# Kernel optimization log

Measured on AMD Instinct MI355X. Metric: run time of the kernel, lower is better.

## Reference

```python
import jax, jax.numpy as jnp
import numpy as np

DIM = 1024
L = 10
C = 1.0
SQRT_C = float(np.sqrt(C))


def _exp_map(x, v, c):
    # Poincare exp map (general form, as in the torch source)
    xn2 = jnp.sum(x * x, axis=-1, keepdims=True)
    lam = 2.0 / (1.0 - c * xn2)
    vn = jnp.sqrt(jnp.sum(v * v, axis=-1, keepdims=True))
    vn = jnp.maximum(vn, 1e-8)
    second = jnp.tanh(SQRT_C * lam * vn / 2.0) / (SQRT_C * vn) * v
    num = (1.0 - c * xn2) * second
    den = (1.0 - 2.0 * c * jnp.sum(x * second, axis=-1, keepdims=True)
           + c * c * xn2 * jnp.sum(second * second, axis=-1, keepdims=True))
    return x + num / den


def _log_map(x, y, c):
    # Poincare log map (general form, as in the torch source)
    xn2 = jnp.sum(x * x, axis=-1, keepdims=True)
    lam = 2.0 / (1.0 - c * xn2)
    yn2 = jnp.sum(y * y, axis=-1, keepdims=True)
    xy = jnp.sum(x * y, axis=-1, keepdims=True)
    tv = (-x * yn2 + y * (1.0 + c * xn2) - 2.0 * c * xy * x) / (1.0 - c * xn2)
    tn = jnp.sqrt(jnp.sum(tv * tv, axis=-1, keepdims=True))
    num = 2.0 * SQRT_C * jnp.arctanh(SQRT_C * tn)
    den = SQRT_C * lam * tn
    return num / den * tv


def _butterfly(u, params):
    # Stage l: blocks of size 2^l along the feature dim; within each block,
    # adjacent pairs are rotated by that block's (a, b) Givens-like rotation.
    # Param layout matches __init__: for layer l there are dim>>l blocks,
    # 2 params (a, b) each, laid out contiguously layer after layer.
    B = u.shape[0]
    offset = 0
    for l in range(L):
        bs = 1 << l
        nb = DIM // bs
        seg = params[offset:offset + 2 * nb]
        offset += 2 * nb
        if bs < 2:
            continue  # block of size 1 has no pair to rotate
        ab = seg.reshape(nb, 2)
        a = ab[:, 0][None, :, None]  # [1, nb, 1]
        b = ab[:, 1][None, :, None]
        u4 = u.reshape(B, nb, bs // 2, 2)
        u0 = u4[..., 0]
        u1 = u4[..., 1]
        u = jnp.stack([a * u0 + b * u1, -b * u0 + a * u1], axis=-1).reshape(B, DIM)
    return u


def setup_inputs() -> dict:
    key = jax.random.key(0)
    k1, k2 = jax.random.split(key)
    # points inside the Poincare ball: per-row norm ~ 0.01*sqrt(1024) ~ 0.32
    x = jax.random.normal(k1, (32768, DIM), dtype=jnp.float32) * 0.01
    P = 2 * sum(DIM >> l for l in range(L))  # 4092
    base = jnp.tile(jnp.array([0.9, 0.0], dtype=jnp.float32), P // 2)
    params = base + 0.1 * jax.random.normal(k2, (P,), dtype=jnp.float32)
    return {"x": x, "params": params}


def reference(x, params):
    u = _log_map(jnp.zeros_like(x), x, C)
    u = _butterfly(u, params)
    return _exp_map(jnp.zeros_like(u), u, C)
```

## Files before the change

kernel.cpp:

```cpp
#include <hip/hip_runtime.h>
#include <math.h>

#define DIM 1024
#define NPAIRS 512
#define NLEVELS 9
#define PAR_OFF (2 * DIM)

__global__ void butterfly_weights_kernel(const float* __restrict__ params,
                                         float2* __restrict__ w) {
#pragma unroll
    for (int h = 0; h < 2; ++h) {
        const int p = threadIdx.x + 256 * h;
        float wr = 1.0f, wi = 0.0f;
        int off = PAR_OFF;
#pragma unroll
        for (int l = 1; l <= NLEVELS; ++l) {
            const int j = p >> (l - 1);
            const float a = params[off + 2 * j];
            const float b = params[off + 2 * j + 1];
            const float nr = wr * a + wi * b;
            const float ni = wi * a - wr * b;
            wr = nr; wi = ni;
            off += 2 * (DIM >> l);
        }
        w[p] = make_float2(wr, wi);
    }
}

__global__ __launch_bounds__(256) void hyper_butterfly_main(
        const float* __restrict__ x,
        const float4* __restrict__ w4,
        float* __restrict__ out,
        int rows) {
    const int lane = threadIdx.x & 63;
    const int wave = threadIdx.x >> 6;
    const int row = blockIdx.x * 4 + wave;
    if (row >= rows) return;

    const float4* xrow = (const float4*)(x + (size_t)row * DIM);
    float4 v[4], W[4];
#pragma unroll
    for (int k = 0; k < 4; ++k) v[k] = xrow[lane + 64 * k];
#pragma unroll
    for (int k = 0; k < 4; ++k) W[k] = w4[lane + 64 * k];

    float xn2 = 0.0f, t = 0.0f;
#pragma unroll
    for (int k = 0; k < 4; ++k) {
        const float n0 = v[k].x * v[k].x + v[k].y * v[k].y;
        const float n1 = v[k].z * v[k].z + v[k].w * v[k].w;
        const float a0 = W[k].x * W[k].x + W[k].y * W[k].y;
        const float a1 = W[k].z * W[k].z + W[k].w * W[k].w;
        xn2 += n0 + n1;
        t   += a0 * n0 + a1 * n1;
    }
#pragma unroll
    for (int m = 32; m > 0; m >>= 1) {
        xn2 += __shfl_xor(xn2, m);
        t   += __shfl_xor(t, m);
    }

    float4 y[4];
#pragma unroll
    for (int k = 0; k < 4; ++k) {
        y[k].x = W[k].x * v[k].x - W[k].y * v[k].y;
        y[k].y = W[k].x * v[k].y + W[k].y * v[k].x;
        y[k].z = W[k].z * v[k].z - W[k].w * v[k].w;
        y[k].w = W[k].z * v[k].w + W[k].w * v[k].z;
    }

    const float r = sqrtf(xn2);
    const float s1 = (r > 1e-12f)
                         ? (0.5f * __logf((1.0f + r) / (1.0f - r)) / r)
                         : 1.0f;
    float vn = fmaxf(s1 * sqrtf(t), 1e-8f);
    float s2;
    if (vn < 1e-4f) {
        s2 = 1.0f - vn * vn * (1.0f / 3.0f);
    } else {
        const float e = __expf(2.0f * vn);
        s2 = (e - 1.0f) / ((e + 1.0f) * vn);
    }
    const float sc = s1 * s2;

    float4* orow = (float4*)(out + (size_t)row * DIM);
#pragma unroll
    for (int k = 0; k < 4; ++k) {
        float4 o;
        o.x = sc * y[k].x; o.y = sc * y[k].y;
        o.z = sc * y[k].z; o.w = sc * y[k].w;
        orow[lane + 64 * k] = o;
    }
}

extern "C" void kernel_launch(void* const* d_in, const int* in_sizes, int n_in,
                              void* d_out, int out_size, void* d_ws, size_t ws_size,
                              hipStream_t stream) {
    const float* x = (const float*)d_in[0];
    const float* params = (const float*)d_in[1];
    float* out = (float*)d_out;
    float2* w = (float2*)d_ws;

    const int rows = in_sizes[0] / DIM;
    const int nblocks = (rows + 3) / 4;

    butterfly_weights_kernel<<<1, 256, 0, stream>>>(params, w);
    hyper_butterfly_main<<<nblocks, 256, 0, stream>>>(x, (const float4*)w, out, rows);
}
```

Baseline: 231.2 us.

## Use persistent grid-stride waves with software prefetch of the next row

Launches a fixed grid of 2048 blocks, each wave looping over rows in grid-stride order. The butterfly weights are loaded once per wave, and the next row's data is prefetched into registers while the current row is reduced and written. This amortizes the weight loads and overlaps global loads with compute, at the cost of higher register pressure and less hardware-level parallelism per row.

```diff
diff --git a/kernel.cpp b/kernel.cpp
--- a/kernel.cpp
+++ b/kernel.cpp
@@ -5,6 +5,7 @@
 #define NPAIRS 512
 #define NLEVELS 9
 #define PAR_OFF (2 * DIM)
+#define NBLOCKS 2048
 
 __global__ void butterfly_weights_kernel(const float* __restrict__ params,
                                          float2* __restrict__ w) {
@@ -27,23 +28,9 @@
     }
 }
 
-__global__ __launch_bounds__(256) void hyper_butterfly_main(
-        const float* __restrict__ x,
-        const float4* __restrict__ w4,
-        float* __restrict__ out,
-        int rows) {
-    const int lane = threadIdx.x & 63;
-    const int wave = threadIdx.x >> 6;
-    const int row = blockIdx.x * 4 + wave;
-    if (row >= rows) return;
-
-    const float4* xrow = (const float4*)(x + (size_t)row * DIM);
-    float4 v[4], W[4];
-#pragma unroll
-    for (int k = 0; k < 4; ++k) v[k] = xrow[lane + 64 * k];
-#pragma unroll
-    for (int k = 0; k < 4; ++k) W[k] = w4[lane + 64 * k];
-
+__device__ __forceinline__ void process_row(
+        const float4 (&v)[4], const float4 (&W)[4],
+        float* __restrict__ out, size_t row, int lane) {
     float xn2 = 0.0f, t = 0.0f;
 #pragma unroll
     for (int k = 0; k < 4; ++k) {
@@ -60,15 +47,6 @@
         t   += __shfl_xor(t, m);
     }
 
-    float4 y[4];
-#pragma unroll
-    for (int k = 0; k < 4; ++k) {
-        y[k].x = W[k].x * v[k].x - W[k].y * v[k].y;
-        y[k].y = W[k].x * v[k].y + W[k].y * v[k].x;
-        y[k].z = W[k].z * v[k].z - W[k].w * v[k].w;
-        y[k].w = W[k].z * v[k].w + W[k].w * v[k].z;
-    }
-
     const float r = sqrtf(xn2);
     const float s1 = (r > 1e-12f)
                          ? (0.5f * __logf((1.0f + r) / (1.0f - r)) / r)
@@ -83,13 +61,58 @@
     }
     const float sc = s1 * s2;
 
-    float4* orow = (float4*)(out + (size_t)row * DIM);
+    float4* orow = (float4*)(out + row * DIM);
 #pragma unroll
     for (int k = 0; k < 4; ++k) {
         float4 o;
-        o.x = sc * y[k].x; o.y = sc * y[k].y;
-        o.z = sc * y[k].z; o.w = sc * y[k].w;
+        o.x = sc * (W[k].x * v[k].x - W[k].y * v[k].y);
+        o.y = sc * (W[k].x * v[k].y + W[k].y * v[k].x);
+        o.z = sc * (W[k].z * v[k].z - W[k].w * v[k].w);
+        o.w = sc * (W[k].z * v[k].w + W[k].w * v[k].z);
         orow[lane + 64 * k] = o;
+    }
+}
+
+__global__ __launch_bounds__(256) void hyper_butterfly_main(
+        const float* __restrict__ x,
+        const float4* __restrict__ w4,
+        float* __restrict__ out,
+        int rows) {
+    const int lane = threadIdx.x & 63;
+    const int wave = threadIdx.x >> 6;
+    const int gwave = blockIdx.x * 4 + wave;
+    const int nwaves = gridDim.x * 4;
+
+    float4 W[4];
+#pragma unroll
+    for (int k = 0; k < 4; ++k) W[k] = w4[lane + 64 * k];
+
+    int row = gwave;
+    if (row >= rows) return;
+
+    float4 v[4];
+    {
+        const float4* xrow = (const float4*)(x + (size_t)row * DIM);
+#pragma unroll
+        for (int k = 0; k < 4; ++k) v[k] = xrow[lane + 64 * k];
+    }
+
+    for (;;) {
+        const int next = row + nwaves;
+        const bool has_next = next < rows;
+        float4 nv[4];
+        if (has_next) {
+            const float4* nxrow = (const float4*)(x + (size_t)next * DIM);
+#pragma unroll
+            for (int k = 0; k < 4; ++k) nv[k] = nxrow[lane + 64 * k];
+        }
+
+        process_row(v, W, out, (size_t)row, lane);
+
+        if (!has_next) break;
+        row = next;
+#pragma unroll
+        for (int k = 0; k < 4; ++k) v[k] = nv[k];
     }
 }
 
@@ -102,7 +125,9 @@
     float2* w = (float2*)d_ws;
 
     const int rows = in_sizes[0] / DIM;
-    const int nblocks = (rows + 3) / 4;
+    int nblocks = NBLOCKS;
+    const int max_needed = (rows + 3) / 4;
+    if (nblocks > max_needed) nblocks = max_needed;
 
     butterfly_weights_kernel<<<1, 256, 0, stream>>>(params, w);
     hyper_butterfly_main<<<nblocks, 256, 0, stream>>>(x, (const float4*)w, out, rows);
```

Result: no change. 233.4 us (+1.0%).
